# Kernel optimization log

Hardware: AMD Instinct MI355X
Metric: run time of the kernel (lower is better)

The kernel has to match this reference:

```python
import jax, jax.numpy as jnp
import numpy as np

N, K, CONV_DIM = 100, 20, 256
TEMP, ALPHA = 0.1, 0.1
B_NORM = 1  # module hardcodes self.B = 1
BATCH = 8


def setup_inputs() -> dict:
    key = jax.random.key(0)
    inputs = jax.random.normal(key, (BATCH, N, K, CONV_DIM), dtype=jnp.float32)
    return {"inputs": inputs}


def reference(inputs) -> jnp.ndarray:
    # inputs: [B, N, K, D] prototype representations
    B, n, k, D = inputs.shape
    # L2-normalize along feature dim (reduce_euclidean_norm)
    xn = inputs / jnp.sqrt(jnp.sum(inputs * inputs, axis=-1, keepdims=True))
    flat = xn.reshape(B, n * k, D)  # all prototypes, all classes: [B, N*K, D]

    # anchor-vs-all similarities: [B, N, K, N*K]
    sims = jnp.einsum('bnkd,bmd->bnkm', xn, flat) / TEMP
    # anchor self-similarity (==1/t after normalization, but keep exact math): [B, N, K]
    self_sim = jnp.sum(xn * xn, axis=-1) / TEMP

    # denominator: sum_m exp(sim) - exp(self)
    denom = jnp.sum(jnp.exp(sims), axis=-1) - jnp.exp(self_sim)
    log_term = jnp.log(denom)  # [B, N, K]

    # intra-class similarity sum: anchor vs all K prototypes of its own class
    intra = jnp.einsum('bnkd,bnjd->bnk', xn, xn) / TEMP  # [B, N, K]
    sum_term = (intra - self_sim) / (k - 1)

    cl_loss = jnp.sum(log_term - sum_term)  # summed over batch and all N*K anchors
    loss = ALPHA * cl_loss / (B_NORM * n * k * D)
    return loss
```

## Files before the change

kernel.cpp:

```cpp
#include <hip/hip_runtime.h>
#include <math.h>

#define BB 8
#define NN 100
#define KK 20
#define DD 256
#define MM 2000
#define MP 2048
#define TINV 10.0f
#define LOSS_SCALE 1.953125e-7f

typedef __bf16 bf16x8 __attribute__((ext_vector_type(8)));
typedef float floatx4 __attribute__((ext_vector_type(4)));
typedef __attribute__((address_space(1))) const ushort GUshort;
typedef __attribute__((address_space(3))) ushort LUshort;

__device__ __forceinline__ ushort f2bf(float f) {
    unsigned int u = __float_as_uint(f);
    u += 0x7fffu + ((u >> 16) & 1u);
    return (ushort)(u >> 16);
}

__global__ void norm_bf16(const float* __restrict__ x, ushort* __restrict__ xb) {
    const int rg = blockIdx.x * 4 + (threadIdx.x >> 6);
    const int lane = threadIdx.x & 63;
    const int b = rg >> 11;
    const int r = rg & (MP - 1);
    ushort4 outv = make_ushort4(0, 0, 0, 0);
    if (r < MM) {
        const float4 v = ((const float4*)(x + ((size_t)(b * MM + r)) * DD))[lane];
        float s = v.x * v.x + v.y * v.y + v.z * v.z + v.w * v.w;
        #pragma unroll
        for (int o = 32; o >= 1; o >>= 1) s += __shfl_xor(s, o, 64);
        const float inv = 1.0f / sqrtf(s);
        outv.x = f2bf(v.x * inv);
        outv.y = f2bf(v.y * inv);
        outv.z = f2bf(v.z * inv);
        outv.w = f2bf(v.w * inv);
    }
    ((ushort4*)(xb + (size_t)rg * DD))[lane] = outv;
}

__global__ __launch_bounds__(256)
void cl_mfma(const ushort* __restrict__ xb,
             float* __restrict__ denom_g, float* __restrict__ intra_g) {
    __shared__ __align__(16) ushort As[128 * 64];
    __shared__ __align__(16) ushort Bs[128 * 64];

    const int b = blockIdx.x / 136;
    int rem = blockIdx.x - b * 136;
    int ti = 0;
    while (rem >= 16 - ti) { rem -= 16 - ti; ++ti; }
    const int tj = ti + rem;
    const int rbase = ti << 7;
    const int cbase = tj << 7;
    const bool offdiag = (ti != tj);
    const ushort* __restrict__ xbb = xb + (size_t)b * MP * DD;

    const int tid = threadIdx.x;
    const int lane = tid & 63;
    const int w = tid >> 6;
    const int wr = (w >> 1) << 6;
    const int wc = (w & 1) << 6;
    const int tx = lane & 15;
    const int tx7 = tx & 7;
    const int quad = lane >> 4;

    const int srow = lane >> 3;
    const int sg = (lane & 7) ^ srow;

    floatx4 acc[4][4];
    #pragma unroll
    for (int mt = 0; mt < 4; ++mt)
        #pragma unroll
        for (int nt = 0; nt < 4; ++nt)
            acc[mt][nt] = (floatx4){0.f, 0.f, 0.f, 0.f};

    #pragma unroll 1
    for (int kc = 0; kc < 4; ++kc) {
        __syncthreads();
        #pragma unroll
        for (int q = 0; q < 4; ++q) {
            const int R = ((w << 2) + q) << 3;
            const size_t koff = (kc << 6) + (sg << 3);
            __builtin_amdgcn_global_load_lds(
                (GUshort*)(xbb + (size_t)(rbase + R + srow) * DD + koff),
                (LUshort*)(As + R * 64), 16, 0, 0);
            __builtin_amdgcn_global_load_lds(
                (GUshort*)(xbb + (size_t)(cbase + R + srow) * DD + koff),
                (LUshort*)(Bs + R * 64), 16, 0, 0);
        }
        __syncthreads();

        #pragma unroll
        for (int ks = 0; ks < 2; ++ks) {
            const int g = (ks << 2) + quad;
            const int gp = (g ^ tx7) << 3;
            bf16x8 af[4], bf[4];
            #pragma unroll
            for (int mt = 0; mt < 4; ++mt)
                af[mt] = *(const bf16x8*)(As + (wr + (mt << 4) + tx) * 64 + gp);
            #pragma unroll
            for (int nt = 0; nt < 4; ++nt)
                bf[nt] = *(const bf16x8*)(Bs + (wc + (nt << 4) + tx) * 64 + gp);
            #pragma unroll
            for (int mt = 0; mt < 4; ++mt)
                #pragma unroll
                for (int nt = 0; nt < 4; ++nt)
                    acc[mt][nt] = __builtin_amdgcn_mfma_f32_16x16x32_bf16(af[mt], bf[nt], acc[mt][nt], 0, 0, 0);
        }
    }

    int colv[4], colcls[4];
    bool colok[4];
    #pragma unroll
    for (int nt = 0; nt < 4; ++nt) {
        const int c = cbase + wc + (nt << 4) + tx;
        colv[nt] = c;
        colok[nt] = c < MM;
        colcls[nt] = c / KK;
    }
    float de_c[4] = {0.f, 0.f, 0.f, 0.f};
    float it_c[4] = {0.f, 0.f, 0.f, 0.f};

    #pragma unroll
    for (int mt = 0; mt < 4; ++mt) {
        #pragma unroll
        for (int i = 0; i < 4; ++i) {
            const int row = rbase + wr + (mt << 4) + (quad << 2) + i;
            const int rcls = row / KK;
            float de = 0.f, it = 0.f;
            #pragma unroll
            for (int nt = 0; nt < 4; ++nt) {
                const float sim = acc[mt][nt][i] * TINV;
                const bool ok = colok[nt] && (colv[nt] != row);
                const float e = ok ? __expf(sim) : 0.0f;
                const float sv = (ok && (colcls[nt] == rcls)) ? sim : 0.0f;
                de += e;
                it += sv;
                de_c[nt] += e;
                it_c[nt] += sv;
            }
            #pragma unroll
            for (int o = 8; o >= 1; o >>= 1) {
                de += __shfl_xor(de, o, 64);
                it += __shfl_xor(it, o, 64);
            }
            if (tx == 0) {
                atomicAdd(&denom_g[b * MP + row], de);
                atomicAdd(&intra_g[b * MP + row], it);
            }
        }
    }

    if (offdiag) {
        #pragma unroll
        for (int nt = 0; nt < 4; ++nt) {
            de_c[nt] += __shfl_xor(de_c[nt], 16, 64);
            de_c[nt] += __shfl_xor(de_c[nt], 32, 64);
            it_c[nt] += __shfl_xor(it_c[nt], 16, 64);
            it_c[nt] += __shfl_xor(it_c[nt], 32, 64);
        }
        if (quad == 0) {
            #pragma unroll
            for (int nt = 0; nt < 4; ++nt) {
                if (colok[nt]) {
                    atomicAdd(&denom_g[b * MP + colv[nt]], de_c[nt]);
                    atomicAdd(&intra_g[b * MP + colv[nt]], it_c[nt]);
                }
            }
        }
    }
}

__global__ void finalize_kernel(const float* __restrict__ denom_g,
                                const float* __restrict__ intra_g,
                                float* __restrict__ out) {
    const int i = blockIdx.x * 256 + threadIdx.x;
    float s = 0.0f;
    if (i < BB * MM) {
        const int b = i / MM;
        const int r = i - b * MM;
        s = logf(denom_g[b * MP + r]) - intra_g[b * MP + r] * (1.0f / (KK - 1));
    }
    #pragma unroll
    for (int o = 32; o >= 1; o >>= 1) s += __shfl_xor(s, o, 64);
    __shared__ float red[4];
    if ((threadIdx.x & 63) == 0) red[threadIdx.x >> 6] = s;
    __syncthreads();
    if (threadIdx.x == 0)
        atomicAdd(out, (red[0] + red[1] + red[2] + red[3]) * LOSS_SCALE);
}

extern "C" void kernel_launch(void* const* d_in, const int* in_sizes, int n_in,
                              void* d_out, int out_size, void* d_ws, size_t ws_size,
                              hipStream_t stream) {
    const float* x = (const float*)d_in[0];
    float* out = (float*)d_out;
    float* denom_g = (float*)d_ws;
    float* intra_g = denom_g + BB * MP;
    ushort* xb = (ushort*)(intra_g + BB * MP);

    hipMemsetAsync(d_ws, 0, (size_t)2 * BB * MP * sizeof(float), stream);
    hipMemsetAsync(d_out, 0, sizeof(float), stream);
    norm_bf16<<<BB * MP / 4, 256, 0, stream>>>(x, xb);
    cl_mfma<<<BB * 136, 256, 0, stream>>>(xb, denom_g, intra_g);
    finalize_kernel<<<(BB * MM + 255) / 256, 256, 0, stream>>>(denom_g, intra_g, out);
}
```

Before: 104.0 us.

## Fuse memsets and finalize into norm and last-block reduction

The two hipMemsetAsync calls are removed: the accumulator buffers and a completion counter are now zeroed inside the normalization kernel. The finalize kernel is folded into the MFMA kernel, where the last block to finish (found via an atomic counter) reduces the log and intra terms and writes the loss. The block-to-tile mapping also interleaves batches so that neighbouring blocks work on different batches. This cuts launch and memset overhead, but the final reduction now runs serially in a single block.

```diff
diff --git a/kernel.cpp b/kernel.cpp
--- a/kernel.cpp
+++ b/kernel.cpp
@@ -7,6 +7,7 @@
 #define DD 256
 #define MM 2000
 #define MP 2048
+#define NTILE 136
 #define TINV 10.0f
 #define LOSS_SCALE 1.953125e-7f
 
@@ -21,7 +22,12 @@
     return (ushort)(u >> 16);
 }
 
-__global__ void norm_bf16(const float* __restrict__ x, ushort* __restrict__ xb) {
+__global__ void norm_bf16(const float* __restrict__ x, ushort* __restrict__ xb,
+                          float* __restrict__ accbuf, unsigned* __restrict__ counter) {
+    if (blockIdx.x < 32)
+        ((float4*)accbuf)[blockIdx.x * 256 + threadIdx.x] = make_float4(0.f, 0.f, 0.f, 0.f);
+    if (blockIdx.x == 0 && threadIdx.x == 0) counter[0] = 0u;
+
     const int rg = blockIdx.x * 4 + (threadIdx.x >> 6);
     const int lane = threadIdx.x & 63;
     const int b = rg >> 11;
@@ -43,12 +49,13 @@
 
 __global__ __launch_bounds__(256)
 void cl_mfma(const ushort* __restrict__ xb,
-             float* __restrict__ denom_g, float* __restrict__ intra_g) {
+             float* __restrict__ denom_g, float* __restrict__ intra_g,
+             unsigned* __restrict__ counter, float* __restrict__ out) {
     __shared__ __align__(16) ushort As[128 * 64];
     __shared__ __align__(16) ushort Bs[128 * 64];
 
-    const int b = blockIdx.x / 136;
-    int rem = blockIdx.x - b * 136;
+    const int b = blockIdx.x & 7;
+    int rem = blockIdx.x >> 3;
     int ti = 0;
     while (rem >= 16 - ti) { rem -= 16 - ti; ++ti; }
     const int tj = ti + rem;
@@ -171,25 +178,32 @@
             }
         }
     }
-}
-
-__global__ void finalize_kernel(const float* __restrict__ denom_g,
-                                const float* __restrict__ intra_g,
-                                float* __restrict__ out) {
-    const int i = blockIdx.x * 256 + threadIdx.x;
-    float s = 0.0f;
-    if (i < BB * MM) {
-        const int b = i / MM;
-        const int r = i - b * MM;
-        s = logf(denom_g[b * MP + r]) - intra_g[b * MP + r] * (1.0f / (KK - 1));
-    }
-    #pragma unroll
-    for (int o = 32; o >= 1; o >>= 1) s += __shfl_xor(s, o, 64);
+
+    __shared__ unsigned lastS;
     __shared__ float red[4];
-    if ((threadIdx.x & 63) == 0) red[threadIdx.x >> 6] = s;
+    __threadfence();
     __syncthreads();
-    if (threadIdx.x == 0)
-        atomicAdd(out, (red[0] + red[1] + red[2] + red[3]) * LOSS_SCALE);
+    if (tid == 0) {
+        const unsigned old = atomicAdd(counter, 1u);
+        lastS = (old == (unsigned)(BB * NTILE - 1)) ? 1u : 0u;
+    }
+    __syncthreads();
+    if (lastS) {
+        __threadfence();
+        float s = 0.0f;
+        for (int i = tid; i < BB * MM; i += 256) {
+            const int bb = i / MM;
+            const int r = i - bb * MM;
+            const float dn = atomicAdd(&denom_g[bb * MP + r], 0.0f);
+            const float it = atomicAdd(&intra_g[bb * MP + r], 0.0f);
+            s += logf(dn) - it * (1.0f / (KK - 1));
+        }
+        #pragma unroll
+        for (int o = 32; o >= 1; o >>= 1) s += __shfl_xor(s, o, 64);
+        if ((tid & 63) == 0) red[tid >> 6] = s;
+        __syncthreads();
+        if (tid == 0) out[0] = (red[0] + red[1] + red[2] + red[3]) * LOSS_SCALE;
+    }
 }
 
 extern "C" void kernel_launch(void* const* d_in, const int* in_sizes, int n_in,
@@ -199,11 +213,9 @@
     float* out = (float*)d_out;
     float* denom_g = (float*)d_ws;
     float* intra_g = denom_g + BB * MP;
-    ushort* xb = (ushort*)(intra_g + BB * MP);
-
-    hipMemsetAsync(d_ws, 0, (size_t)2 * BB * MP * sizeof(float), stream);
-    hipMemsetAsync(d_out, 0, sizeof(float), stream);
-    norm_bf16<<<BB * MP / 4, 256, 0, stream>>>(x, xb);
-    cl_mfma<<<BB * 136, 256, 0, stream>>>(xb, denom_g, intra_g);
-    finalize_kernel<<<(BB * MM + 255) / 256, 256, 0, stream>>>(denom_g, intra_g, out);
-}
+    unsigned* counter = (unsigned*)(intra_g + BB * MP);
+    ushort* xb = (ushort*)((char*)d_ws + (size_t)2 * BB * MP * sizeof(float) + 256);
+
+    norm_bf16<<<BB * MP / 4, 256, 0, stream>>>(x, xb, denom_g, counter);
+    cl_mfma<<<BB * NTILE, 256, 0, stream>>>(xb, denom_g, intra_g, counter, out);
+}
```

Measured after the change: 180.8 us. +73.9%, slower.
